# Performance work log

Hardware: AMD Instinct MI355X
Metric: run time of the kernel (lower is better)

The kernel has to match this reference:

```python
import jax, jax.numpy as jnp
import numpy as np

NUM_CAPSULE = 64
DIM_CAPSULE = 128
ROUTINGS = 3
EPS = 1e-7  # K.epsilon()


def squash(s, axis=-1):
    sq_norm = jnp.sum(jnp.square(s), axis=axis, keepdims=True) + EPS
    scale = jnp.sqrt(sq_norm) / (0.5 + sq_norm)
    return scale * s


def setup_inputs() -> dict:
    key = jax.random.key(0)
    k1, k2 = jax.random.split(key)
    B, N_IN, D_IN = 16, 512, 256
    x = jax.random.normal(k1, (B, N_IN, D_IN), dtype=jnp.float32)
    # glorot-uniform kernel (flattened conv1d kernel of shape (1, D_IN, NC*DC))
    fan_out = NUM_CAPSULE * DIM_CAPSULE
    limit = float(np.sqrt(6.0 / (D_IN + fan_out)))
    kernel = jax.random.uniform(k2, (D_IN, fan_out), dtype=jnp.float32,
                                minval=-limit, maxval=limit)
    return {"x": x, "kernel": kernel}


def reference(x, kernel):
    B, N, _ = x.shape
    # conv1d with kernel_size=1 == matmul over last dim
    hat = jnp.einsum('bni,io->bno', x, kernel)
    hat = hat.reshape(B, N, NUM_CAPSULE, DIM_CAPSULE).transpose(0, 2, 1, 3)  # [B, C, N, D]
    b = jnp.zeros((B, NUM_CAPSULE, N), dtype=hat.dtype)
    o = None
    for i in range(ROUTINGS):
        c = jax.nn.softmax(b, axis=1)  # softmax over output capsules (axis 1)
        o = squash(jnp.einsum('bcn,bcnd->bcd', c, hat))  # [B, C, D]
        if i < ROUTINGS - 1:
            b = b + jnp.einsum('bcd,bcnd->bcn', o, hat)
    return o
```

## Files before the change

kernel.cpp:

```cpp
#include <hip/hip_runtime.h>
#include <hip/hip_bf16.h>

#define NB 16
#define NN 512
#define DI 256
#define NC 64
#define ND 128
#define FO 8192
#define NP 8

typedef __attribute__((ext_vector_type(8))) short short8v;
typedef __attribute__((ext_vector_type(4))) short short4v;
typedef __attribute__((ext_vector_type(4))) float f32x4;
typedef unsigned short us16;

__device__ __forceinline__ us16 f2b(float f) {
  union { __hip_bfloat16 h; us16 u; } cv; cv.h = __float2bfloat16(f); return cv.u;
}
__device__ __forceinline__ float b2f(us16 u) {
  union { unsigned u; float f; } cv; cv.u = ((unsigned)u) << 16; return cv.f;
}

__global__ __launch_bounds__(256) void k_pre(const float* __restrict__ x,
                                             const float* __restrict__ kern,
                                             us16* __restrict__ khT,
                                             us16* __restrict__ kh,
                                             us16* __restrict__ xh,
                                             us16* __restrict__ xhT,
                                             float* __restrict__ xsum_p) {
  int task = blockIdx.x;
  int tid = threadIdx.x;

  if (task < 512) {
    int c = task >> 3, i0 = (task & 7) * 32;
    __shared__ float buf[32][129];
#pragma unroll
    for (int k = 0; k < 4; ++k) {
      int e4 = tid + k * 256;
      int r = e4 >> 5, dq = e4 & 31;
      float4 v = *(const float4*)(kern + (size_t)(i0 + r) * FO + c * ND + dq * 4);
      buf[r][dq * 4 + 0] = v.x; buf[r][dq * 4 + 1] = v.y;
      buf[r][dq * 4 + 2] = v.z; buf[r][dq * 4 + 3] = v.w;
    }
    __syncthreads();
#pragma unroll
    for (int k = 0; k < 16; ++k) {
      int e = tid + k * 256;
      int il = e & 31, d = e >> 5;
      khT[((size_t)c * ND + d) * DI + i0 + il] = f2b(buf[il][d]);
    }
    {
      int r = tid >> 3, dg = (tid & 7) * 16;
      us16 tmp[16];
#pragma unroll
      for (int e = 0; e < 16; ++e) tmp[e] = f2b(buf[r][dg + e]);
      us16* dst = kh + (size_t)(i0 + r) * FO + c * ND + dg;
      *(short8v*)dst = *(short8v*)tmp;
      *(short8v*)(dst + 8) = *(short8v*)(tmp + 8);
    }
  } else if (task < 1024) {
    int idx = task - 512;
    int b = idx >> 5, rem = idx & 31;
    int nb = (rem >> 2) * 64, ib = (rem & 3) * 64;
    __shared__ float buf2[64][68];
#pragma unroll
    for (int k = 0; k < 4; ++k) {
      int e4 = tid + k * 256;
      int nl = e4 >> 4, q4 = e4 & 15;
      float4 v = *(const float4*)(x + ((size_t)b * NN + nb + nl) * DI + ib + q4 * 4);
      *(float4*)&buf2[nl][q4 * 4] = v;
    }
    __syncthreads();
    {
      int nl = tid >> 2, ig = (tid & 3) * 16;
      us16 tmp[16];
#pragma unroll
      for (int e = 0; e < 16; ++e) tmp[e] = f2b(buf2[nl][ig + e]);
      us16* dst = xh + ((size_t)b * NN + nb + nl) * DI + ib + ig;
      *(short8v*)dst = *(short8v*)tmp;
      *(short8v*)(dst + 8) = *(short8v*)(tmp + 8);
    }
    {
      int il = tid & 63, ng = tid >> 6;
      us16 tmp[16];
#pragma unroll
      for (int e = 0; e < 16; ++e) tmp[e] = f2b(buf2[ng * 16 + e][il]);
      us16* dst = xhT + ((size_t)b * DI + ib + il) * NN + nb + ng * 16;
      *(short8v*)dst = *(short8v*)tmp;
      *(short8v*)(dst + 8) = *(short8v*)(tmp + 8);
    }
  } else {
    int idx = task - 1024;
    int b = idx >> 2, q = idx & 3;
    int ns = tid >> 6, i4 = tid & 63;
    float4 a = {0.f, 0.f, 0.f, 0.f};
    const float4* xp = (const float4*)(x + ((size_t)b * NN + q * 128 + ns * 32) * DI) + i4;
#pragma unroll 4
    for (int n = 0; n < 32; ++n) {
      float4 v = xp[(size_t)n * 64];
      a.x += v.x; a.y += v.y; a.z += v.z; a.w += v.w;
    }
    __shared__ float4 red[4][64];
    red[ns][i4] = a;
    __syncthreads();
    if (ns == 0) {
      float4 s0 = red[0][i4], s1 = red[1][i4], s2 = red[2][i4], s3 = red[3][i4];
      float4 s;
      s.x = s0.x + s1.x + s2.x + s3.x;  s.y = s0.y + s1.y + s2.y + s3.y;
      s.z = s0.z + s1.z + s2.z + s3.z;  s.w = s0.w + s1.w + s2.w + s3.w;
      ((float4*)(xsum_p + ((size_t)q * NB + b) * DI))[i4] = s;
    }
  }
}

template <int MODE>
__global__ __launch_bounds__(512) void k_owm(const us16* __restrict__ khT,
                                             const us16* __restrict__ kh,
                                             const us16* __restrict__ yp_in,
                                             const float* __restrict__ xsum_p,
                                             us16* __restrict__ whc,
                                             float* __restrict__ outp) {
  int c = blockIdx.x;
  int tid = threadIdx.x;
  int lane = tid & 63, w = tid >> 6;
  int m16 = lane & 15, ko = lane >> 4;

  __shared__ us16 ybf[16 * 256];
  __shared__ us16 ob[16 * 128];
  __shared__ float o_f32[16][132];

  {
    int b = tid >> 5, u = tid & 31;
    int i8 = u * 8;
    float v[8];
#pragma unroll
    for (int e = 0; e < 8; ++e) v[e] = 0.f;
    if constexpr (MODE == 0) {
#pragma unroll
      for (int q = 0; q < 4; ++q) {
        const float* sp = xsum_p + ((size_t)q * NB + b) * DI + i8;
        float4 a = *(const float4*)sp;
        float4 d = *(const float4*)(sp + 4);
        v[0] += a.x; v[1] += a.y; v[2] += a.z; v[3] += a.w;
        v[4] += d.x; v[5] += d.y; v[6] += d.z; v[7] += d.w;
      }
#pragma unroll
      for (int e = 0; e < 8; ++e) v[e] *= (1.f / 64.f);
    } else {
      const us16* base = yp_in + ((size_t)b * NC + c) * DI + i8;
#pragma unroll
      for (int p = 0; p < NP; ++p) {
        short8v t = *(const short8v*)(base + (size_t)p * (NB * NC * DI));
#pragma unroll
        for (int e = 0; e < 8; ++e) v[e] += b2f((us16)t[e]);
      }
    }
    us16 tmp[8];
#pragma unroll
    for (int e = 0; e < 8; ++e) tmp[e] = f2b(v[e]);
    *(short8v*)&ybf[b * 256 + ((u ^ (b & 7)) * 8)] = *(short8v*)tmp;
  }
  __syncthreads();

  {
    int d0 = w * 16;
    f32x4 acc = {0.f, 0.f, 0.f, 0.f};
#pragma unroll
    for (int kk = 0; kk < 8; ++kk) {
      int kb = kk * 4 + ko;
      short8v av = *(const short8v*)&ybf[m16 * 256 + ((kb ^ (m16 & 7)) * 8)];
      short8v bv = *(const short8v*)(khT + ((size_t)c * ND + d0 + m16) * DI + kk * 32 + ko * 8);
      acc = __builtin_amdgcn_mfma_f32_16x16x32_bf16(av, bv, acc, 0, 0, 0);
    }
#pragma unroll
    for (int r = 0; r < 4; ++r) o_f32[ko * 4 + r][d0 + m16] = acc[r];
  }
  __syncthreads();

  {
    int b = tid >> 5, j = tid & 31;
    float4 o = *(const float4*)&o_f32[b][j * 4];
    float sq = o.x * o.x + o.y * o.y + o.z * o.z + o.w * o.w;
#pragma unroll
    for (int off = 16; off >= 1; off >>= 1) sq += __shfl_xor(sq, off, 64);
    float tot = sq + 1e-7f;
    float scale = sqrtf(tot) / (0.5f + tot);
    o.x *= scale; o.y *= scale; o.z *= scale; o.w *= scale;
    if constexpr (MODE == 2) {
      ((float4*)(outp + ((size_t)b * NC + c) * ND))[j] = o;
    } else {
      us16 tmp[4] = {f2b(o.x), f2b(o.y), f2b(o.z), f2b(o.w)};
      *(short4v*)&ob[b * 128 + (((j >> 1) ^ (b & 7)) * 8) + (j & 1) * 4] = *(short4v*)tmp;
    }
  }
  __syncthreads();

  if constexpr (MODE < 2) {
#pragma unroll
    for (int nt = 0; nt < 2; ++nt) {
      int i0 = (w * 2 + nt) * 16;
      f32x4 acc = {0.f, 0.f, 0.f, 0.f};
#pragma unroll
      for (int kk = 0; kk < 4; ++kk) {
        int kb = kk * 4 + ko;
        short8v av = *(const short8v*)&ob[m16 * 128 + ((kb ^ (m16 & 7)) * 8)];
        short8v bv = *(const short8v*)(kh + (size_t)(i0 + m16) * FO + c * ND + kk * 32 + ko * 8);
        acc = __builtin_amdgcn_mfma_f32_16x16x32_bf16(av, bv, acc, 0, 0, 0);
      }
#pragma unroll
      for (int r = 0; r < 4; ++r)
        whc[((size_t)(ko * 4 + r) * NC + c) * DI + i0 + m16] = f2b(acc[r]);
    }
  }
}

template <bool ADD_B, bool STORE_B>
__global__ __launch_bounds__(512) void k_sy(const us16* __restrict__ xh,
                                            const us16* __restrict__ xhT,
                                            const us16* __restrict__ whc,
                                            float* __restrict__ blog,
                                            us16* __restrict__ y_p) {
  int b = blockIdx.x, p = blockIdx.y;
  int tid = threadIdx.x;
  int lane = tid & 63, w = tid >> 6;
  int m16 = lane & 15, ko = lane >> 4;
  int n0 = p * 64;

  __shared__ float s_lds[64][65];
  __shared__ us16 cT[64][72];

  {
    int Mt = w & 3;
#pragma unroll
    for (int t = 0; t < 2; ++t) {
      int Nt = (w >> 2) * 2 + t;
      const us16* wrow = whc + ((size_t)b * NC + Mt * 16 + m16) * DI + ko * 8;
      const us16* xrow = xh + ((size_t)b * NN + n0 + Nt * 16 + m16) * DI + ko * 8;
      f32x4 acc = {0.f, 0.f, 0.f, 0.f};
#pragma unroll
      for (int k8 = 0; k8 < 8; ++k8) {
        short8v av = *(const short8v*)(wrow + k8 * 32);
        short8v bv = *(const short8v*)(xrow + k8 * 32);
        acc = __builtin_amdgcn_mfma_f32_16x16x32_bf16(av, bv, acc, 0, 0, 0);
      }
#pragma unroll
      for (int r = 0; r < 4; ++r)
        s_lds[Nt * 16 + m16][Mt * 16 + ko * 4 + r] = acc[r];
    }
  }
  __syncthreads();

  {
    us16 pk[8];
#pragma unroll
    for (int nn = 0; nn < 8; ++nn) {
      int n = w * 8 + nn;
      float v = s_lds[n][lane];
      size_t gi = ((size_t)b * NN + n0 + n) * NC + lane;
      if (ADD_B) v += blog[gi];
      if (STORE_B) blog[gi] = v;
      float m = v;
#pragma unroll
      for (int off = 32; off >= 1; off >>= 1) m = fmaxf(m, __shfl_xor(m, off, 64));
      float e = __expf(v - m);
      float s = e;
#pragma unroll
      for (int off = 32; off >= 1; off >>= 1) s += __shfl_xor(s, off, 64);
      pk[nn] = f2b(e / s);
    }
    *(short8v*)&cT[lane][w * 8] = *(short8v*)pk;
  }
  __syncthreads();

  {
    int Mt2 = w & 3;
    short8v a0 = *(const short8v*)&cT[Mt2 * 16 + m16][ko * 8];
    short8v a1 = *(const short8v*)&cT[Mt2 * 16 + m16][32 + ko * 8];
    us16* yb = y_p + ((size_t)p * NB + b) * (NC * DI);
#pragma unroll
    for (int q = 0; q < 8; ++q) {
      int it = (w >> 2) * 8 + q;
      const us16* xr = xhT + ((size_t)b * DI + it * 16 + m16) * NN + n0;
      f32x4 acc = {0.f, 0.f, 0.f, 0.f};
      short8v bv0 = *(const short8v*)(xr + ko * 8);
      short8v bv1 = *(const short8v*)(xr + 32 + ko * 8);
      acc = __builtin_amdgcn_mfma_f32_16x16x32_bf16(a0, bv0, acc, 0, 0, 0);
      acc = __builtin_amdgcn_mfma_f32_16x16x32_bf16(a1, bv1, acc, 0, 0, 0);
#pragma unroll
      for (int r = 0; r < 4; ++r)
        yb[(size_t)(Mt2 * 16 + ko * 4 + r) * DI + it * 16 + m16] = f2b(acc[r]);
    }
  }
}

extern "C" void kernel_launch(void* const* d_in, const int* in_sizes, int n_in,
                              void* d_out, int out_size, void* d_ws, size_t ws_size,
                              hipStream_t stream) {
  (void)in_sizes; (void)n_in; (void)out_size; (void)ws_size;
  const float* x    = (const float*)d_in[0];
  const float* kern = (const float*)d_in[1];
  float* out = (float*)d_out;

  char* wp = (char*)d_ws;
  us16* khT  = (us16*)wp;  wp += (size_t)NC * ND * DI * 2;
  us16* kh   = (us16*)wp;  wp += (size_t)DI * FO * 2;
  us16* xh   = (us16*)wp;  wp += (size_t)NB * NN * DI * 2;
  us16* xhT  = (us16*)wp;  wp += (size_t)NB * DI * NN * 2;
  us16* whc  = (us16*)wp;  wp += (size_t)NB * NC * DI * 2;
  us16* y_p  = (us16*)wp;  wp += (size_t)NP * NB * NC * DI * 2;
  float* blog   = (float*)wp;  wp += (size_t)NB * NN * NC * 4;
  float* xsum_p = (float*)wp;

  k_pre<<<1088, 256, 0, stream>>>(x, kern, khT, kh, xh, xhT, xsum_p);

  k_owm<0><<<NC, 512, 0, stream>>>(khT, kh, y_p, xsum_p, whc, nullptr);
  k_sy<false, true><<<dim3(NB, NP), 512, 0, stream>>>(xh, xhT, whc, blog, y_p);
  k_owm<1><<<NC, 512, 0, stream>>>(khT, kh, y_p, xsum_p, whc, nullptr);
  k_sy<true, false><<<dim3(NB, NP), 512, 0, stream>>>(xh, xhT, whc, blog, y_p);
  k_owm<2><<<NC, 512, 0, stream>>>(khT, kh, y_p, xsum_p, whc, out);
}
```

Before: 63.55 us.

## Split routing kernels across more blocks and fuse x-sum into conversion pass

The routing-logit kernel now handles 32 input positions per block instead of 64, doubling the partial count to 16 and launching twice as many blocks. The capsule-output kernel is split over batch groups of four (grid 64x4, 256 threads), zero-padding the MFMA M dimension. The separate x column-sum blocks are removed and folded into the x bf16 conversion tiles via LDS. This aims to raise parallelism across CUs in the small-grid kernels, at the cost of wasted MFMA lanes on padded rows and more partial-sum reads.

```diff
diff --git a/kernel.cpp b/kernel.cpp
--- a/kernel.cpp
+++ b/kernel.cpp
@@ -7,7 +7,7 @@
 #define NC 64
 #define ND 128
 #define FO 8192
-#define NP 8
+#define NP 16
 
 typedef __attribute__((ext_vector_type(8))) short short8v;
 typedef __attribute__((ext_vector_type(4))) short short4v;
@@ -27,7 +27,7 @@
                                              us16* __restrict__ kh,
                                              us16* __restrict__ xh,
                                              us16* __restrict__ xhT,
-                                             float* __restrict__ xsum_p) {
+                                             float* __restrict__ xsum_pp) {
   int task = blockIdx.x;
   int tid = threadIdx.x;
 
@@ -58,11 +58,13 @@
       *(short8v*)dst = *(short8v*)tmp;
       *(short8v*)(dst + 8) = *(short8v*)(tmp + 8);
     }
-  } else if (task < 1024) {
+  } else {
     int idx = task - 512;
     int b = idx >> 5, rem = idx & 31;
-    int nb = (rem >> 2) * 64, ib = (rem & 3) * 64;
+    int nq = rem >> 2, ib = (rem & 3) * 64;
+    int nb = nq * 64;
     __shared__ float buf2[64][68];
+    __shared__ float red[4][64];
 #pragma unroll
     for (int k = 0; k < 4; ++k) {
       int e4 = tid + k * 256;
@@ -89,97 +91,88 @@
       *(short8v*)dst = *(short8v*)tmp;
       *(short8v*)(dst + 8) = *(short8v*)(tmp + 8);
     }
-  } else {
-    int idx = task - 1024;
-    int b = idx >> 2, q = idx & 3;
-    int ns = tid >> 6, i4 = tid & 63;
-    float4 a = {0.f, 0.f, 0.f, 0.f};
-    const float4* xp = (const float4*)(x + ((size_t)b * NN + q * 128 + ns * 32) * DI) + i4;
-#pragma unroll 4
-    for (int n = 0; n < 32; ++n) {
-      float4 v = xp[(size_t)n * 64];
-      a.x += v.x; a.y += v.y; a.z += v.z; a.w += v.w;
-    }
-    __shared__ float4 red[4][64];
-    red[ns][i4] = a;
+    {
+      int il = tid & 63, rg = tid >> 6;
+      float s = 0.f;
+#pragma unroll
+      for (int r = 0; r < 16; ++r) s += buf2[rg * 16 + r][il];
+      red[rg][il] = s;
+    }
     __syncthreads();
-    if (ns == 0) {
-      float4 s0 = red[0][i4], s1 = red[1][i4], s2 = red[2][i4], s3 = red[3][i4];
-      float4 s;
-      s.x = s0.x + s1.x + s2.x + s3.x;  s.y = s0.y + s1.y + s2.y + s3.y;
-      s.z = s0.z + s1.z + s2.z + s3.z;  s.w = s0.w + s1.w + s2.w + s3.w;
-      ((float4*)(xsum_p + ((size_t)q * NB + b) * DI))[i4] = s;
-    }
+    if (tid < 64)
+      xsum_pp[((size_t)nq * NB + b) * DI + ib + tid] =
+          red[0][tid] + red[1][tid] + red[2][tid] + red[3][tid];
   }
 }
 
 template <int MODE>
-__global__ __launch_bounds__(512) void k_owm(const us16* __restrict__ khT,
+__global__ __launch_bounds__(256) void k_owm(const us16* __restrict__ khT,
                                              const us16* __restrict__ kh,
                                              const us16* __restrict__ yp_in,
-                                             const float* __restrict__ xsum_p,
+                                             const float* __restrict__ xsum_pp,
                                              us16* __restrict__ whc,
                                              float* __restrict__ outp) {
-  int c = blockIdx.x;
+  int c = blockIdx.x, b0 = blockIdx.y * 4;
   int tid = threadIdx.x;
   int lane = tid & 63, w = tid >> 6;
   int m16 = lane & 15, ko = lane >> 4;
 
   __shared__ us16 ybf[16 * 256];
-  __shared__ us16 ob[16 * 128];
-  __shared__ float o_f32[16][132];
-
-  {
-    int b = tid >> 5, u = tid & 31;
-    int i8 = u * 8;
-    float v[8];
-#pragma unroll
-    for (int e = 0; e < 8; ++e) v[e] = 0.f;
+  __shared__ float o_f32[4][132];
+  __shared__ us16 ob[4 * 128];
+
+  {
+    int bb = tid >> 6, u4 = tid & 63;
+    float4 v;
     if constexpr (MODE == 0) {
-#pragma unroll
-      for (int q = 0; q < 4; ++q) {
-        const float* sp = xsum_p + ((size_t)q * NB + b) * DI + i8;
-        float4 a = *(const float4*)sp;
-        float4 d = *(const float4*)(sp + 4);
-        v[0] += a.x; v[1] += a.y; v[2] += a.z; v[3] += a.w;
-        v[4] += d.x; v[5] += d.y; v[6] += d.z; v[7] += d.w;
-      }
-#pragma unroll
-      for (int e = 0; e < 8; ++e) v[e] *= (1.f / 64.f);
+      v.x = v.y = v.z = v.w = 0.f;
+#pragma unroll
+      for (int q = 0; q < 8; ++q) {
+        float4 t = ((const float4*)(xsum_pp + ((size_t)q * NB + b0 + bb) * DI))[u4];
+        v.x += t.x; v.y += t.y; v.z += t.z; v.w += t.w;
+      }
+      v.x *= (1.f / 64.f); v.y *= (1.f / 64.f); v.z *= (1.f / 64.f); v.w *= (1.f / 64.f);
     } else {
-      const us16* base = yp_in + ((size_t)b * NC + c) * DI + i8;
+      float a0 = 0.f, a1 = 0.f, a2 = 0.f, a3 = 0.f;
+      const us16* base = yp_in + ((size_t)(b0 + bb) * NC + c) * DI + u4 * 4;
 #pragma unroll
       for (int p = 0; p < NP; ++p) {
-        short8v t = *(const short8v*)(base + (size_t)p * (NB * NC * DI));
-#pragma unroll
-        for (int e = 0; e < 8; ++e) v[e] += b2f((us16)t[e]);
-      }
-    }
-    us16 tmp[8];
-#pragma unroll
-    for (int e = 0; e < 8; ++e) tmp[e] = f2b(v[e]);
-    *(short8v*)&ybf[b * 256 + ((u ^ (b & 7)) * 8)] = *(short8v*)tmp;
-  }
-  __syncthreads();
-
-  {
-    int d0 = w * 16;
-    f32x4 acc = {0.f, 0.f, 0.f, 0.f};
-#pragma unroll
-    for (int kk = 0; kk < 8; ++kk) {
-      int kb = kk * 4 + ko;
-      short8v av = *(const short8v*)&ybf[m16 * 256 + ((kb ^ (m16 & 7)) * 8)];
-      short8v bv = *(const short8v*)(khT + ((size_t)c * ND + d0 + m16) * DI + kk * 32 + ko * 8);
-      acc = __builtin_amdgcn_mfma_f32_16x16x32_bf16(av, bv, acc, 0, 0, 0);
-    }
-#pragma unroll
-    for (int r = 0; r < 4; ++r) o_f32[ko * 4 + r][d0 + m16] = acc[r];
-  }
-  __syncthreads();
-
-  {
-    int b = tid >> 5, j = tid & 31;
-    float4 o = *(const float4*)&o_f32[b][j * 4];
+        short4v t = *(const short4v*)(base + (size_t)p * (NB * NC * DI));
+        a0 += b2f((us16)t[0]); a1 += b2f((us16)t[1]);
+        a2 += b2f((us16)t[2]); a3 += b2f((us16)t[3]);
+      }
+      v.x = a0; v.y = a1; v.z = a2; v.w = a3;
+    }
+    us16 tmp[4] = {f2b(v.x), f2b(v.y), f2b(v.z), f2b(v.w)};
+    *(short4v*)&ybf[bb * 256 + (((u4 >> 1) ^ bb) * 8) + (u4 & 1) * 4] = *(short4v*)tmp;
+#pragma unroll
+    for (int r = 0; r < 12; ++r) ybf[(4 + r) * 256 + tid] = 0;
+  }
+  __syncthreads();
+
+  {
+#pragma unroll
+    for (int nt = 0; nt < 2; ++nt) {
+      int d0 = (w * 2 + nt) * 16;
+      f32x4 acc = {0.f, 0.f, 0.f, 0.f};
+#pragma unroll
+      for (int kk = 0; kk < 8; ++kk) {
+        int kb = kk * 4 + ko;
+        short8v av = *(const short8v*)&ybf[m16 * 256 + ((kb ^ (m16 & 7)) * 8)];
+        short8v bv = *(const short8v*)(khT + ((size_t)c * ND + d0 + m16) * DI + kk * 32 + ko * 8);
+        acc = __builtin_amdgcn_mfma_f32_16x16x32_bf16(av, bv, acc, 0, 0, 0);
+      }
+      if (ko == 0) {
+#pragma unroll
+        for (int r = 0; r < 4; ++r) o_f32[r][d0 + m16] = acc[r];
+      }
+    }
+  }
+  __syncthreads();
+
+  if (tid < 128) {
+    int bb = tid >> 5, j = tid & 31;
+    float4 o = *(const float4*)&o_f32[bb][j * 4];
     float sq = o.x * o.x + o.y * o.y + o.z * o.z + o.w * o.w;
 #pragma unroll
     for (int off = 16; off >= 1; off >>= 1) sq += __shfl_xor(sq, off, 64);
@@ -187,29 +180,31 @@
     float scale = sqrtf(tot) / (0.5f + tot);
     o.x *= scale; o.y *= scale; o.z *= scale; o.w *= scale;
     if constexpr (MODE == 2) {
-      ((float4*)(outp + ((size_t)b * NC + c) * ND))[j] = o;
+      ((float4*)(outp + ((size_t)(b0 + bb) * NC + c) * ND))[j] = o;
     } else {
       us16 tmp[4] = {f2b(o.x), f2b(o.y), f2b(o.z), f2b(o.w)};
-      *(short4v*)&ob[b * 128 + (((j >> 1) ^ (b & 7)) * 8) + (j & 1) * 4] = *(short4v*)tmp;
+      *(short4v*)&ob[bb * 128 + (((j >> 1) ^ bb) * 8) + (j & 1) * 4] = *(short4v*)tmp;
     }
   }
   __syncthreads();
 
   if constexpr (MODE < 2) {
 #pragma unroll
-    for (int nt = 0; nt < 2; ++nt) {
-      int i0 = (w * 2 + nt) * 16;
+    for (int nt = 0; nt < 4; ++nt) {
+      int i0 = (w * 4 + nt) * 16;
       f32x4 acc = {0.f, 0.f, 0.f, 0.f};
 #pragma unroll
       for (int kk = 0; kk < 4; ++kk) {
         int kb = kk * 4 + ko;
-        short8v av = *(const short8v*)&ob[m16 * 128 + ((kb ^ (m16 & 7)) * 8)];
+        short8v av = *(const short8v*)&ob[(m16 & 3) * 128 + ((kb ^ (m16 & 3)) * 8)];
         short8v bv = *(const short8v*)(kh + (size_t)(i0 + m16) * FO + c * ND + kk * 32 + ko * 8);
         acc = __builtin_amdgcn_mfma_f32_16x16x32_bf16(av, bv, acc, 0, 0, 0);
       }
-#pragma unroll
-      for (int r = 0; r < 4; ++r)
-        whc[((size_t)(ko * 4 + r) * NC + c) * DI + i0 + m16] = f2b(acc[r]);
+      if (ko == 0) {
+#pragma unroll
+        for (int r = 0; r < 4; ++r)
+          whc[((size_t)(b0 + r) * NC + c) * DI + i0 + m16] = f2b(acc[r]);
+      }
     }
   }
 }
@@ -224,37 +219,33 @@
   int tid = threadIdx.x;
   int lane = tid & 63, w = tid >> 6;
   int m16 = lane & 15, ko = lane >> 4;
-  int n0 = p * 64;
-
-  __shared__ float s_lds[64][65];
-  __shared__ us16 cT[64][72];
-
-  {
-    int Mt = w & 3;
-#pragma unroll
-    for (int t = 0; t < 2; ++t) {
-      int Nt = (w >> 2) * 2 + t;
-      const us16* wrow = whc + ((size_t)b * NC + Mt * 16 + m16) * DI + ko * 8;
-      const us16* xrow = xh + ((size_t)b * NN + n0 + Nt * 16 + m16) * DI + ko * 8;
-      f32x4 acc = {0.f, 0.f, 0.f, 0.f};
-#pragma unroll
-      for (int k8 = 0; k8 < 8; ++k8) {
-        short8v av = *(const short8v*)(wrow + k8 * 32);
-        short8v bv = *(const short8v*)(xrow + k8 * 32);
-        acc = __builtin_amdgcn_mfma_f32_16x16x32_bf16(av, bv, acc, 0, 0, 0);
-      }
-#pragma unroll
-      for (int r = 0; r < 4; ++r)
-        s_lds[Nt * 16 + m16][Mt * 16 + ko * 4 + r] = acc[r];
-    }
-  }
-  __syncthreads();
-
-  {
-    us16 pk[8];
-#pragma unroll
-    for (int nn = 0; nn < 8; ++nn) {
-      int n = w * 8 + nn;
+  int n0 = p * 32;
+
+  __shared__ float s_lds[32][65];
+  __shared__ us16 cT[64][40];
+
+  {
+    int Mt = w & 3, Nt = w >> 2;
+    const us16* wrow = whc + ((size_t)b * NC + Mt * 16 + m16) * DI + ko * 8;
+    const us16* xrow = xh + ((size_t)b * NN + n0 + Nt * 16 + m16) * DI + ko * 8;
+    f32x4 acc = {0.f, 0.f, 0.f, 0.f};
+#pragma unroll
+    for (int k8 = 0; k8 < 8; ++k8) {
+      short8v av = *(const short8v*)(wrow + k8 * 32);
+      short8v bv = *(const short8v*)(xrow + k8 * 32);
+      acc = __builtin_amdgcn_mfma_f32_16x16x32_bf16(av, bv, acc, 0, 0, 0);
+    }
+#pragma unroll
+    for (int r = 0; r < 4; ++r)
+      s_lds[Nt * 16 + m16][Mt * 16 + ko * 4 + r] = acc[r];
+  }
+  __syncthreads();
+
+  {
+    us16 pk[4];
+#pragma unroll
+    for (int nn = 0; nn < 4; ++nn) {
+      int n = w * 4 + nn;
       float v = s_lds[n][lane];
       size_t gi = ((size_t)b * NN + n0 + n) * NC + lane;
       if (ADD_B) v += blog[gi];
@@ -268,28 +259,35 @@
       for (int off = 32; off >= 1; off >>= 1) s += __shfl_xor(s, off, 64);
       pk[nn] = f2b(e / s);
     }
-    *(short8v*)&cT[lane][w * 8] = *(short8v*)pk;
-  }
-  __syncthreads();
-
-  {
-    int Mt2 = w & 3;
-    short8v a0 = *(const short8v*)&cT[Mt2 * 16 + m16][ko * 8];
-    short8v a1 = *(const short8v*)&cT[Mt2 * 16 + m16][32 + ko * 8];
+    *(short4v*)&cT[lane][w * 4] = *(short4v*)pk;
+  }
+  __syncthreads();
+
+  {
+    int Mp = w >> 2, Ng = w & 3;
+    short8v a0 = *(const short8v*)&cT[(Mp * 2 + 0) * 16 + m16][ko * 8];
+    short8v a1 = *(const short8v*)&cT[(Mp * 2 + 1) * 16 + m16][ko * 8];
+    f32x4 acc[2][4];
+#pragma unroll
+    for (int t = 0; t < 2; ++t)
+#pragma unroll
+      for (int q = 0; q < 4; ++q) { acc[t][q][0]=acc[t][q][1]=acc[t][q][2]=acc[t][q][3]=0.f; }
+#pragma unroll
+    for (int q = 0; q < 4; ++q) {
+      int icol = (Ng * 4 + q) * 16 + m16;
+      short8v bv = *(const short8v*)(xhT + ((size_t)b * DI + icol) * NN + n0 + ko * 8);
+      acc[0][q] = __builtin_amdgcn_mfma_f32_16x16x32_bf16(a0, bv, acc[0][q], 0, 0, 0);
+      acc[1][q] = __builtin_amdgcn_mfma_f32_16x16x32_bf16(a1, bv, acc[1][q], 0, 0, 0);
+    }
     us16* yb = y_p + ((size_t)p * NB + b) * (NC * DI);
 #pragma unroll
-    for (int q = 0; q < 8; ++q) {
-      int it = (w >> 2) * 8 + q;
-      const us16* xr = xhT + ((size_t)b * DI + it * 16 + m16) * NN + n0;
-      f32x4 acc = {0.f, 0.f, 0.f, 0.f};
-      short8v bv0 = *(const short8v*)(xr + ko * 8);
-      short8v bv1 = *(const short8v*)(xr + 32 + ko * 8);
-      acc = __builtin_amdgcn_mfma_f32_16x16x32_bf16(a0, bv0, acc, 0, 0, 0);
-      acc = __builtin_amdgcn_mfma_f32_16x16x32_bf16(a1, bv1, acc, 0, 0, 0);
-#pragma unroll
-      for (int r = 0; r < 4; ++r)
-        yb[(size_t)(Mt2 * 16 + ko * 4 + r) * DI + it * 16 + m16] = f2b(acc[r]);
-    }
+    for (int t = 0; t < 2; ++t)
+#pragma unroll
+      for (int q = 0; q < 4; ++q)
+#pragma unroll
+        for (int r = 0; r < 4; ++r)
+          yb[(size_t)((Mp * 2 + t) * 16 + ko * 4 + r) * DI + (Ng * 4 + q) * 16 + m16] =
+              f2b(acc[t][q][r]);
   }
 }
 
@@ -308,14 +306,14 @@
   us16* xhT  = (us16*)wp;  wp += (size_t)NB * DI * NN * 2;
   us16* whc  = (us16*)wp;  wp += (size_t)NB * NC * DI * 2;
   us16* y_p  = (us16*)wp;  wp += (size_t)NP * NB * NC * DI * 2;
-  float* blog   = (float*)wp;  wp += (size_t)NB * NN * NC * 4;
-  float* xsum_p = (float*)wp;
-
-  k_pre<<<1088, 256, 0, stream>>>(x, kern, khT, kh, xh, xhT, xsum_p);
-
-  k_owm<0><<<NC, 512, 0, stream>>>(khT, kh, y_p, xsum_p, whc, nullptr);
+  float* blog    = (float*)wp;  wp += (size_t)NB * NN * NC * 4;
+  float* xsum_pp = (float*)wp;
+
+  k_pre<<<1024, 256, 0, stream>>>(x, kern, khT, kh, xh, xhT, xsum_pp);
+
+  k_owm<0><<<dim3(NC, 4), 256, 0, stream>>>(khT, kh, y_p, xsum_pp, whc, nullptr);
   k_sy<false, true><<<dim3(NB, NP), 512, 0, stream>>>(xh, xhT, whc, blog, y_p);
-  k_owm<1><<<NC, 512, 0, stream>>>(khT, kh, y_p, xsum_p, whc, nullptr);
+  k_owm<1><<<dim3(NC, 4), 256, 0, stream>>>(khT, kh, y_p, xsum_pp, whc, nullptr);
   k_sy<true, false><<<dim3(NB, NP), 512, 0, stream>>>(xh, xhT, whc, blog, y_p);
-  k_owm<2><<<NC, 512, 0, stream>>>(khT, kh, y_p, xsum_p, whc, out);
-}
+  k_owm<2><<<dim3(NC, 4), 256, 0, stream>>>(khT, kh, y_p, xsum_pp, whc, out);
+}
```

Measured after the change: 55.87 us. -12.1%, faster.
